# Optimization experiments

Hardware: AMD Instinct MI355X
Metric: run time of the kernel (lower is better)

Reference implementation:

```python
import jax, jax.numpy as jnp
import numpy as np

DIM = 192
NUM_HEADS = 6
WIN = (2, 7, 7)


def _relative_position_index(win):
    d, h, w = win
    coords = np.stack(np.meshgrid(np.arange(d), np.arange(h), np.arange(w), indexing='ij'))
    cf = coords.reshape(3, -1)  # (3, n)
    rel = cf[:, :, None] - cf[:, None, :]  # (3, n, n)
    rel = rel.transpose(1, 2, 0).copy()
    rel[:, :, 0] += d - 1
    rel[:, :, 1] += h - 1
    rel[:, :, 2] += w - 1
    rel[:, :, 0] *= (2 * h - 1) * (2 * w - 1)
    rel[:, :, 1] *= 2 * w - 1
    return rel.sum(-1).astype(np.int32)  # (n, n)


def setup_inputs() -> dict:
    key = jax.random.key(0)
    ks = jax.random.split(key, 8)
    n = WIN[0] * WIN[1] * WIN[2]  # 98
    table_size = (2 * WIN[0] - 1) * (2 * WIN[1] - 1) * (2 * WIN[2] - 1)  # 507
    b_ = 4096
    nW = 64
    x = jax.random.normal(ks[0], (b_, n, DIM), dtype=jnp.float32)
    mask = jax.random.normal(ks[1], (nW, n, n), dtype=jnp.float32)
    qkv_w = jax.random.normal(ks[2], (3 * DIM, DIM), dtype=jnp.float32) * (DIM ** -0.5)
    qkv_b = jnp.zeros((3 * DIM,), dtype=jnp.float32)
    proj_w = jax.random.normal(ks[3], (DIM, DIM), dtype=jnp.float32) * (DIM ** -0.5)
    proj_b = jnp.zeros((DIM,), dtype=jnp.float32)
    rpb_table = jax.random.normal(ks[4], (table_size, NUM_HEADS), dtype=jnp.float32) * 0.02
    rel_idx = jnp.asarray(_relative_position_index(WIN))  # (n, n) int32
    return {"x": x, "mask": mask, "qkv_w": qkv_w, "qkv_b": qkv_b,
            "proj_w": proj_w, "proj_b": proj_b, "rpb_table": rpb_table,
            "rel_idx": rel_idx}


def reference(x, mask, qkv_w, qkv_b, proj_w, proj_b, rpb_table, rel_idx):
    b_, n, c = x.shape
    H = NUM_HEADS
    hd = c // H
    scale = hd ** -0.5
    # QKV projection: (b_, n, 3, H, hd) -> (3, b_, H, n, hd)
    qkv = (x @ qkv_w.T + qkv_b).reshape(b_, n, 3, H, hd).transpose(2, 0, 3, 1, 4)
    q, k, v = qkv[0] * scale, qkv[1], qkv[2]
    attn = jnp.einsum('bhnd,bhmd->bhnm', q, k)
    # relative position bias gathered per (n, n) pair -> (H, n, n)
    bias = rpb_table[rel_idx]  # (n, n, H)
    attn = attn + bias.transpose(2, 0, 1)[None]
    # window mask add
    nW = mask.shape[0]
    attn = attn.reshape(b_ // nW, nW, H, n, n) + mask[None, :, None]
    attn = attn.reshape(b_, H, n, n)
    attn = jax.nn.softmax(attn, axis=-1)
    out = jnp.einsum('bhnm,bhmd->bhnd', attn, v)
    out = out.transpose(0, 2, 1, 3).reshape(b_, n, c)
    return out @ proj_w.T + proj_b
```

## Files before the change

### kernel.cpp

```cpp
#include <hip/hip_runtime.h>
#include <hip/hip_bf16.h>

#define NN 98
#define CC 192
#define NH 6
#define HDIM 32
#define NWIN 64
#define MPAD 100
#define NSTR 200
#define SWS 1920

#define WKV_ELEMS 73728
#define WQ_ELEMS  36864
#define WP_ELEMS  36864

typedef float f32x4 __attribute__((ext_vector_type(4)));
typedef __bf16 bf16x8 __attribute__((ext_vector_type(8)));
typedef __bf16 bf16x4 __attribute__((ext_vector_type(4)));

__device__ __forceinline__ f32x4 mfma_bf16(bf16x8 a, bf16x8 b, f32x4 c) {
  return __builtin_amdgcn_mfma_f32_16x16x32_bf16(a, b, c, 0, 0, 0);
}

__device__ __forceinline__ bf16x8 zero8() {
  bf16x8 z;
#pragma unroll
  for (int i = 0; i < 8; ++i) z[i] = (__bf16)0.0f;
  return z;
}

__device__ __forceinline__ float fast_exp2(float x) {
#if __has_builtin(__builtin_amdgcn_exp2f)
  return __builtin_amdgcn_exp2f(x);
#else
  return exp2f(x);
#endif
}

__device__ __forceinline__ bf16x8 ldlds8(const __bf16* p, int row, int k0) {
  int rc = row < NN ? row : (NN - 1);
  bf16x8 v = *(const bf16x8*)(p + rc * NSTR + k0);
  if (row >= NN) v = zero8();
  return v;
}

__global__ void prep_kernel(const float* __restrict__ mask,
                            const float* __restrict__ rpb,
                            const int* __restrict__ rel_idx,
                            const float* __restrict__ qkv_w,
                            const float* __restrict__ proj_w,
                            float* __restrict__ biasp,
                            float* __restrict__ maskp,
                            __bf16* __restrict__ wkvp,
                            __bf16* __restrict__ wqp,
                            __bf16* __restrict__ wpp) {
  const float LOG2E = 1.4426950408889634f;
  int i = blockIdx.x * 256 + threadIdx.x;
  if (i < NH * NN * MPAD) {
    int m = i % MPAD;
    int rem = i / MPAD;
    int n = rem % NN;
    int h = rem / NN;
    biasp[i] = (m < NN) ? rpb[rel_idx[n * NN + m] * NH + h] * LOG2E : -1e30f;
  }
  if (i < NWIN * NN * MPAD) {
    int m = i % MPAD;
    int rem = i / MPAD;
    int n = rem % NN;
    int wi = rem / NN;
    maskp[i] = (m < NN) ? mask[(wi * NN + n) * NN + m] * LOG2E : -1e30f;
  }
  if (i < WKV_ELEMS) {
    int j = i & 7;
    int lane = (i >> 3) & 63;
    int f = (i >> 9) & 3;
    int t = i >> 11;
    int ks = t % 6;
    int w = t / 6;
    int l15 = lane & 15, quad = lane >> 4;
    int row = (f < 2 ? CC : 2 * CC) + w * HDIM + (f & 1) * 16 + l15;
    int col = ks * 32 + quad * 8 + j;
    wkvp[i] = (__bf16)qkv_w[row * CC + col];
  }
  if (i < WQ_ELEMS) {
    int j = i & 7;
    int lane = (i >> 3) & 63;
    int f = (i >> 9) & 1;
    int t = i >> 10;
    int ks = t % 6;
    int w = t / 6;
    int l15 = lane & 15, quad = lane >> 4;
    int row = w * HDIM + f * 16 + l15;
    int col = ks * 32 + quad * 8 + j;
    wqp[i] = (__bf16)qkv_w[row * CC + col];
    wpp[i] = (__bf16)proj_w[row * CC + col];
  }
}

__global__ __launch_bounds__(384, 3) void attn_kernel(
    const float* __restrict__ x,
    const float* __restrict__ qkv_b,
    const float* __restrict__ proj_b,
    const float* __restrict__ biasp,
    const float* __restrict__ maskp,
    const __bf16* __restrict__ wkvp,
    const __bf16* __restrict__ wqp,
    const __bf16* __restrict__ wpp,
    float* __restrict__ out) {
  __shared__ alignas(16) __bf16 xs[NN * NSTR];
  __shared__ alignas(16) __bf16 stage[NH * SWS];

  const int b = blockIdx.x;
  const int tid = threadIdx.x;
  const int w = tid >> 6;
  const int lane = tid & 63;
  const int l15 = lane & 15;
  const int quad = lane >> 4;
  __bf16* st = stage + w * SWS;

  const float* xb = x + (size_t)b * (NN * CC);
  for (int i = tid; i < NN * CC / 4; i += 384) {
    int e = i * 4;
    int n = e / CC;
    int c = e - n * CC;
    f32x4 v = *(const f32x4*)(xb + e);
    bf16x4 p;
    p[0] = (__bf16)v[0]; p[1] = (__bf16)v[1]; p[2] = (__bf16)v[2]; p[3] = (__bf16)v[3];
    *(bf16x4*)&xs[n * NSTR + c] = p;
  }
  __syncthreads();

  f32x4 acc[2][7];

#pragma unroll
  for (int ct = 0; ct < 2; ++ct) {
    float bb = qkv_b[CC + w * HDIM + ct * 16 + l15];
#pragma unroll
    for (int rt = 0; rt < 7; ++rt) { f32x4 t = {bb, bb, bb, bb}; acc[ct][rt] = t; }
  }
  {
    const __bf16* wb = wkvp + (size_t)(w * 24) * 512 + lane * 8;
#pragma unroll
    for (int ks = 0; ks < 6; ++ks) {
      bf16x8 b0 = *(const bf16x8*)(wb + (ks * 4 + 0) * 512);
      bf16x8 b1 = *(const bf16x8*)(wb + (ks * 4 + 1) * 512);
      const int k0 = ks * 32 + quad * 8;
#pragma unroll
      for (int rt = 0; rt < 7; ++rt) {
        bf16x8 a = ldlds8(xs, rt * 16 + l15, k0);
        acc[0][rt] = mfma_bf16(a, b0, acc[0][rt]);
        acc[1][rt] = mfma_bf16(a, b1, acc[1][rt]);
      }
    }
  }

  bf16x8 ka[7];
#pragma unroll
  for (int rt = 0; rt < 7; ++rt) {
#pragma unroll
    for (int ct = 0; ct < 2; ++ct) {
      f32x4 v = acc[ct][rt];
      int hd = ct * 16 + l15;
#pragma unroll
      for (int r = 0; r < 4; ++r) st[(quad * 4 + r) * 40 + hd] = (__bf16)v[r];
    }
    bf16x8 f = *(const bf16x8*)&st[l15 * 40 + quad * 8];
    if (rt * 16 + l15 >= NN) f = zero8();
    ka[rt] = f;
  }

#pragma unroll
  for (int ct = 0; ct < 2; ++ct) {
    float bb = qkv_b[2 * CC + w * HDIM + ct * 16 + l15];
#pragma unroll
    for (int rt = 0; rt < 7; ++rt) { f32x4 t = {bb, bb, bb, bb}; acc[ct][rt] = t; }
  }
  {
    const __bf16* wb = wkvp + (size_t)(w * 24) * 512 + lane * 8;
#pragma unroll
    for (int ks = 0; ks < 6; ++ks) {
      bf16x8 b0 = *(const bf16x8*)(wb + (ks * 4 + 2) * 512);
      bf16x8 b1 = *(const bf16x8*)(wb + (ks * 4 + 3) * 512);
      const int k0 = ks * 32 + quad * 8;
#pragma unroll
      for (int rt = 0; rt < 7; ++rt) {
        bf16x8 a = ldlds8(xs, rt * 16 + l15, k0);
        acc[0][rt] = mfma_bf16(a, b0, acc[0][rt]);
        acc[1][rt] = mfma_bf16(a, b1, acc[1][rt]);
      }
    }
  }

  bf16x8 va[2][4];
#pragma unroll
  for (int ks = 0; ks < 4; ++ks) {
#pragma unroll
    for (int h2 = 0; h2 < 2; ++h2) {
      int rt = 2 * ks + h2;
      if (rt < 7) {
#pragma unroll
        for (int ct = 0; ct < 2; ++ct) {
          f32x4 v = acc[ct][rt];
          int d = ct * 16 + l15;
          int mloc = h2 * 16 + quad * 4;
          bf16x4 p;
#pragma unroll
          for (int r = 0; r < 4; ++r) p[r] = (__bf16)v[r];
          *(bf16x4*)&st[d * 40 + mloc] = p;
        }
      }
    }
#pragma unroll
    for (int dt = 0; dt < 2; ++dt) {
      bf16x8 f = *(const bf16x8*)&st[(dt * 16 + l15) * 40 + quad * 8];
      if (ks == 3 && quad >= 2) f = zero8();
      va[dt][ks] = f;
    }
  }

#pragma unroll
  for (int ct = 0; ct < 2; ++ct) {
    float bq = qkv_b[w * HDIM + ct * 16 + l15];
#pragma unroll
    for (int rt = 0; rt < 7; ++rt) { f32x4 t = {bq, bq, bq, bq}; acc[ct][rt] = t; }
  }
  {
    const __bf16* wb = wqp + (size_t)(w * 12) * 512 + lane * 8;
#pragma unroll
    for (int ks = 0; ks < 6; ++ks) {
      bf16x8 b0 = *(const bf16x8*)(wb + (ks * 2 + 0) * 512);
      bf16x8 b1 = *(const bf16x8*)(wb + (ks * 2 + 1) * 512);
      const int k0 = ks * 32 + quad * 8;
#pragma unroll
      for (int rt = 0; rt < 7; ++rt) {
        bf16x8 a = ldlds8(xs, rt * 16 + l15, k0);
        acc[0][rt] = mfma_bf16(a, b0, acc[0][rt]);
        acc[1][rt] = mfma_bf16(a, b1, acc[1][rt]);
      }
    }
  }

  const float qscale = 0.17677669529663687f * 1.4426950408889634f;
  bf16x8 qb[7];
#pragma unroll
  for (int rt = 0; rt < 7; ++rt) {
#pragma unroll
    for (int ct = 0; ct < 2; ++ct) {
      f32x4 v = acc[ct][rt];
      int hd = ct * 16 + l15;
#pragma unroll
      for (int r = 0; r < 4; ++r) st[(quad * 4 + r) * 40 + hd] = (__bf16)(v[r] * qscale);
    }
    bf16x8 f = *(const bf16x8*)&st[l15 * 40 + quad * 8];
    if (rt * 16 + l15 >= NN) f = zero8();
    qb[rt] = f;
  }

  __syncthreads();
  __bf16* O_lds = xs;

  const int wmask = b & (NWIN - 1);
#pragma unroll 1
  for (int nb = 0; nb < 7; ++nb) {
    const f32x4 z4 = {0.f, 0.f, 0.f, 0.f};
    f32x4 sacc[7];
#pragma unroll
    for (int mt = 0; mt < 7; ++mt) sacc[mt] = mfma_bf16(ka[mt], qb[nb], z4);

    int n = nb * 16 + l15;
    bool nvalid = (n < NN);
    int nc = nvalid ? n : 0;
    const float* bp = biasp + (size_t)(w * NN + nc) * MPAD;
    const float* mp = maskp + (size_t)(wmask * NN + nc) * MPAD;

    float mx = -3.0e38f;
#pragma unroll
    for (int mt = 0; mt < 7; ++mt) {
      int m0 = mt * 16 + quad * 4;
      bool ld = nvalid && (m0 < MPAD);
      f32x4 add = z4;
      if (ld) {
        f32x4 bm = *(const f32x4*)(bp + m0);
        f32x4 mm = *(const f32x4*)(mp + m0);
        add = bm + mm;
      }
#pragma unroll
      for (int r = 0; r < 4; ++r) {
        float v = ld ? (sacc[mt][r] + add[r]) : -1e30f;
        sacc[mt][r] = v;
        mx = fmaxf(mx, v);
      }
    }
    mx = fmaxf(mx, __shfl_xor(mx, 16, 64));
    mx = fmaxf(mx, __shfl_xor(mx, 32, 64));
    float sum = 0.f;
#pragma unroll
    for (int mt = 0; mt < 7; ++mt) {
#pragma unroll
      for (int r = 0; r < 4; ++r) {
        float p = fast_exp2(sacc[mt][r] - mx);
        sacc[mt][r] = p;
        sum += p;
      }
    }
    sum += __shfl_xor(sum, 16, 64);
    sum += __shfl_xor(sum, 32, 64);
    float rinv = 1.0f / sum;

#pragma unroll
    for (int mt = 0; mt < 7; ++mt) {
      bf16x4 p;
#pragma unroll
      for (int r = 0; r < 4; ++r) p[r] = (__bf16)sacc[mt][r];
      *(bf16x4*)&st[l15 * 120 + mt * 16 + quad * 4] = p;
    }
    bf16x8 pf[4];
#pragma unroll
    for (int ks = 0; ks < 4; ++ks) {
      bf16x8 f = *(const bf16x8*)&st[l15 * 120 + ks * 32 + quad * 8];
      if (ks == 3 && quad >= 2) f = zero8();
      pf[ks] = f;
    }

#pragma unroll
    for (int dt = 0; dt < 2; ++dt) {
      f32x4 o = z4;
#pragma unroll
      for (int ks = 0; ks < 4; ++ks) o = mfma_bf16(va[dt][ks], pf[ks], o);
      if (nvalid) {
        bf16x4 p;
#pragma unroll
        for (int r = 0; r < 4; ++r) p[r] = (__bf16)(o[r] * rinv);
        *(bf16x4*)&O_lds[n * NSTR + w * HDIM + dt * 16 + quad * 4] = p;
      }
    }
  }
  __syncthreads();

  f32x4 accP[2][7];
#pragma unroll
  for (int ct = 0; ct < 2; ++ct) {
    float pb = proj_b[w * HDIM + ct * 16 + l15];
#pragma unroll
    for (int rt = 0; rt < 7; ++rt) { f32x4 t = {pb, pb, pb, pb}; accP[ct][rt] = t; }
  }
  {
    const __bf16* wb = wpp + (size_t)(w * 12) * 512 + lane * 8;
#pragma unroll
    for (int ks = 0; ks < 6; ++ks) {
      bf16x8 b0 = *(const bf16x8*)(wb + (ks * 2 + 0) * 512);
      bf16x8 b1 = *(const bf16x8*)(wb + (ks * 2 + 1) * 512);
      const int k0 = ks * 32 + quad * 8;
#pragma unroll
      for (int rt = 0; rt < 7; ++rt) {
        bf16x8 a = ldlds8(O_lds, rt * 16 + l15, k0);
        accP[0][rt] = mfma_bf16(a, b0, accP[0][rt]);
        accP[1][rt] = mfma_bf16(a, b1, accP[1][rt]);
      }
    }
  }

  float* ob = out + (size_t)b * (NN * CC);
#pragma unroll
  for (int ct = 0; ct < 2; ++ct) {
    int cout = w * HDIM + ct * 16 + l15;
#pragma unroll
    for (int rt = 0; rt < 7; ++rt) {
      f32x4 v = accP[ct][rt];
#pragma unroll
      for (int r = 0; r < 4; ++r) {
        int n = rt * 16 + quad * 4 + r;
        if (n < NN) ob[n * CC + cout] = v[r];
      }
    }
  }
}

extern "C" void kernel_launch(void* const* d_in, const int* in_sizes, int n_in,
                              void* d_out, int out_size, void* d_ws, size_t ws_size,
                              hipStream_t stream) {
  const float* x = (const float*)d_in[0];
  const float* mask = (const float*)d_in[1];
  const float* qkv_w = (const float*)d_in[2];
  const float* qkv_b = (const float*)d_in[3];
  const float* proj_w = (const float*)d_in[4];
  const float* proj_b = (const float*)d_in[5];
  const float* rpb = (const float*)d_in[6];
  const int* rel_idx = (const int*)d_in[7];

  float* biasp = (float*)d_ws;
  float* maskp = biasp + NH * NN * MPAD;
  __bf16* wkvp = (__bf16*)(maskp + NWIN * NN * MPAD);
  __bf16* wqp = wkvp + WKV_ELEMS;
  __bf16* wpp = wqp + WQ_ELEMS;

  int prep_threads = NWIN * NN * MPAD;
  prep_kernel<<<(prep_threads + 255) / 256, 256, 0, stream>>>(
      mask, rpb, rel_idx, qkv_w, proj_w, biasp, maskp, wkvp, wqp, wpp);
  attn_kernel<<<4096, 384, 0, stream>>>(x, qkv_b, proj_b, biasp, maskp,
                                        wkvp, wqp, wpp, (float*)d_out);
}
```

Measured before the change: 1.562 ms.

## Pre-swizzle x into MFMA fragment layout and merge bias+mask table

Result: slower. 1.757 ms (+12.5%).

```diff
diff --git a/kernel.cpp b/kernel.cpp
--- a/kernel.cpp
+++ b/kernel.cpp
@@ -9,10 +9,12 @@
 #define MPAD 100
 #define NSTR 200
 #define SWS 1920
+#define NB 4096
 
 #define WKV_ELEMS 73728
 #define WQ_ELEMS  36864
-#define WP_ELEMS  36864
+#define COMB_ELEMS (NWIN * NH * NN * MPAD)
+#define XT_ELEMS ((size_t)NB * 42 * 512)
 
 typedef float f32x4 __attribute__((ext_vector_type(4)));
 typedef __bf16 bf16x8 __attribute__((ext_vector_type(8)));
@@ -37,38 +39,42 @@
 #endif
 }
 
-__device__ __forceinline__ bf16x8 ldlds8(const __bf16* p, int row, int k0) {
+__device__ __forceinline__ bf16x8 ldw8(const float* __restrict__ p) {
+  f32x4 a = *(const f32x4*)p;
+  f32x4 b = *(const f32x4*)(p + 4);
+  bf16x8 r;
+  r[0] = (__bf16)a[0]; r[1] = (__bf16)a[1]; r[2] = (__bf16)a[2]; r[3] = (__bf16)a[3];
+  r[4] = (__bf16)b[0]; r[5] = (__bf16)b[1]; r[6] = (__bf16)b[2]; r[7] = (__bf16)b[3];
+  return r;
+}
+
+__device__ __forceinline__ bf16x8 ldo(const __bf16* p, int row, int k0) {
   int rc = row < NN ? row : (NN - 1);
-  bf16x8 v = *(const bf16x8*)(p + rc * NSTR + k0);
-  if (row >= NN) v = zero8();
-  return v;
-}
-
-__global__ void prep_kernel(const float* __restrict__ mask,
-                            const float* __restrict__ rpb,
-                            const int* __restrict__ rel_idx,
-                            const float* __restrict__ qkv_w,
-                            const float* __restrict__ proj_w,
-                            float* __restrict__ biasp,
-                            float* __restrict__ maskp,
-                            __bf16* __restrict__ wkvp,
-                            __bf16* __restrict__ wqp,
-                            __bf16* __restrict__ wpp) {
+  return *(const bf16x8*)(p + rc * NSTR + k0);
+}
+
+__global__ void prep_small(const float* __restrict__ mask,
+                           const float* __restrict__ rpb,
+                           const int* __restrict__ rel_idx,
+                           const float* __restrict__ qkv_w,
+                           const float* __restrict__ proj_w,
+                           float* __restrict__ comb,
+                           __bf16* __restrict__ wkvp,
+                           __bf16* __restrict__ wqp,
+                           __bf16* __restrict__ wpp) {
   const float LOG2E = 1.4426950408889634f;
   int i = blockIdx.x * 256 + threadIdx.x;
-  if (i < NH * NN * MPAD) {
+  if (i < COMB_ELEMS) {
     int m = i % MPAD;
     int rem = i / MPAD;
     int n = rem % NN;
-    int h = rem / NN;
-    biasp[i] = (m < NN) ? rpb[rel_idx[n * NN + m] * NH + h] * LOG2E : -1e30f;
-  }
-  if (i < NWIN * NN * MPAD) {
-    int m = i % MPAD;
-    int rem = i / MPAD;
-    int n = rem % NN;
-    int wi = rem / NN;
-    maskp[i] = (m < NN) ? mask[(wi * NN + n) * NN + m] * LOG2E : -1e30f;
+    int rem2 = rem / NN;
+    int h = rem2 % NH;
+    int wi = rem2 / NH;
+    float v = -1e30f;
+    if (m < NN)
+      v = (rpb[rel_idx[n * NN + m] * NH + h] + mask[((size_t)wi * NN + n) * NN + m]) * LOG2E;
+    comb[i] = v;
   }
   if (i < WKV_ELEMS) {
     int j = i & 7;
@@ -97,17 +103,38 @@
   }
 }
 
+__global__ void prep_x(const float* __restrict__ x, __bf16* __restrict__ xt) {
+  int t = blockIdx.x * 256 + threadIdx.x;
+  int lane = t & 63;
+  int fid = t >> 6;
+  int rt = fid % 7;
+  int rem = fid / 7;
+  int ks = rem % 6;
+  int b = rem / 6;
+  int l15 = lane & 15, quad = lane >> 4;
+  int n = rt * 16 + l15;
+  bf16x8 v;
+  if (n < NN) {
+    const float* p = x + ((size_t)b * NN + n) * CC + ks * 32 + quad * 8;
+    v = ldw8(p);
+  } else {
+    v = zero8();
+  }
+  *(bf16x8*)&xt[(size_t)fid * 512 + lane * 8] = v;
+}
+
+template <bool XT>
 __global__ __launch_bounds__(384, 3) void attn_kernel(
     const float* __restrict__ x,
     const float* __restrict__ qkv_b,
     const float* __restrict__ proj_b,
-    const float* __restrict__ biasp,
-    const float* __restrict__ maskp,
+    const float* __restrict__ comb,
     const __bf16* __restrict__ wkvp,
     const __bf16* __restrict__ wqp,
     const __bf16* __restrict__ wpp,
+    const __bf16* __restrict__ xt,
     float* __restrict__ out) {
-  __shared__ alignas(16) __bf16 xs[NN * NSTR];
+  __shared__ alignas(16) __bf16 O_lds[NN * NSTR];
   __shared__ alignas(16) __bf16 stage[NH * SWS];
 
   const int b = blockIdx.x;
@@ -117,18 +144,8 @@
   const int l15 = lane & 15;
   const int quad = lane >> 4;
   __bf16* st = stage + w * SWS;
-
+  const __bf16* xtb = xt + (size_t)b * (42 * 512);
   const float* xb = x + (size_t)b * (NN * CC);
-  for (int i = tid; i < NN * CC / 4; i += 384) {
-    int e = i * 4;
-    int n = e / CC;
-    int c = e - n * CC;
-    f32x4 v = *(const f32x4*)(xb + e);
-    bf16x4 p;
-    p[0] = (__bf16)v[0]; p[1] = (__bf16)v[1]; p[2] = (__bf16)v[2]; p[3] = (__bf16)v[3];
-    *(bf16x4*)&xs[n * NSTR + c] = p;
-  }
-  __syncthreads();
 
   f32x4 acc[2][7];
 
@@ -144,10 +161,15 @@
     for (int ks = 0; ks < 6; ++ks) {
       bf16x8 b0 = *(const bf16x8*)(wb + (ks * 4 + 0) * 512);
       bf16x8 b1 = *(const bf16x8*)(wb + (ks * 4 + 1) * 512);
-      const int k0 = ks * 32 + quad * 8;
 #pragma unroll
       for (int rt = 0; rt < 7; ++rt) {
-        bf16x8 a = ldlds8(xs, rt * 16 + l15, k0);
+        bf16x8 a;
+        if (XT) {
+          a = *(const bf16x8*)&xtb[(ks * 7 + rt) * 512 + lane * 8];
+        } else {
+          int n = rt * 16 + l15;
+          a = (n < NN) ? ldw8(xb + n * CC + ks * 32 + quad * 8) : zero8();
+        }
         acc[0][rt] = mfma_bf16(a, b0, acc[0][rt]);
         acc[1][rt] = mfma_bf16(a, b1, acc[1][rt]);
       }
@@ -164,9 +186,7 @@
 #pragma unroll
       for (int r = 0; r < 4; ++r) st[(quad * 4 + r) * 40 + hd] = (__bf16)v[r];
     }
-    bf16x8 f = *(const bf16x8*)&st[l15 * 40 + quad * 8];
-    if (rt * 16 + l15 >= NN) f = zero8();
-    ka[rt] = f;
+    ka[rt] = *(const bf16x8*)&st[l15 * 40 + quad * 8];
   }
 
 #pragma unroll
@@ -181,10 +201,15 @@
     for (int ks = 0; ks < 6; ++ks) {
       bf16x8 b0 = *(const bf16x8*)(wb + (ks * 4 + 2) * 512);
       bf16x8 b1 = *(const bf16x8*)(wb + (ks * 4 + 3) * 512);
-      const int k0 = ks * 32 + quad * 8;
 #pragma unroll
       for (int rt = 0; rt < 7; ++rt) {
-        bf16x8 a = ldlds8(xs, rt * 16 + l15, k0);
+        bf16x8 a;
+        if (XT) {
+          a = *(const bf16x8*)&xtb[(ks * 7 + rt) * 512 + lane * 8];
+        } else {
+          int n = rt * 16 + l15;
+          a = (n < NN) ? ldw8(xb + n * CC + ks * 32 + quad * 8) : zero8();
+        }
         acc[0][rt] = mfma_bf16(a, b0, acc[0][rt]);
         acc[1][rt] = mfma_bf16(a, b1, acc[1][rt]);
       }
@@ -230,10 +255,15 @@
     for (int ks = 0; ks < 6; ++ks) {
       bf16x8 b0 = *(const bf16x8*)(wb + (ks * 2 + 0) * 512);
       bf16x8 b1 = *(const bf16x8*)(wb + (ks * 2 + 1) * 512);
-      const int k0 = ks * 32 + quad * 8;
 #pragma unroll
       for (int rt = 0; rt < 7; ++rt) {
-        bf16x8 a = ldlds8(xs, rt * 16 + l15, k0);
+        bf16x8 a;
+        if (XT) {
+          a = *(const bf16x8*)&xtb[(ks * 7 + rt) * 512 + lane * 8];
+        } else {
+          int n = rt * 16 + l15;
+          a = (n < NN) ? ldw8(xb + n * CC + ks * 32 + quad * 8) : zero8();
+        }
         acc[0][rt] = mfma_bf16(a, b0, acc[0][rt]);
         acc[1][rt] = mfma_bf16(a, b1, acc[1][rt]);
       }
@@ -251,42 +281,38 @@
 #pragma unroll
       for (int r = 0; r < 4; ++r) st[(quad * 4 + r) * 40 + hd] = (__bf16)(v[r] * qscale);
     }
-    bf16x8 f = *(const bf16x8*)&st[l15 * 40 + quad * 8];
-    if (rt * 16 + l15 >= NN) f = zero8();
-    qb[rt] = f;
-  }
-
-  __syncthreads();
-  __bf16* O_lds = xs;
+    qb[rt] = *(const bf16x8*)&st[l15 * 40 + quad * 8];
+  }
 
   const int wmask = b & (NWIN - 1);
+  const float* cbase = comb + (size_t)(wmask * NH + w) * NN * MPAD;
 #pragma unroll 1
   for (int nb = 0; nb < 7; ++nb) {
     const f32x4 z4 = {0.f, 0.f, 0.f, 0.f};
-    f32x4 sacc[7];
-#pragma unroll
-    for (int mt = 0; mt < 7; ++mt) sacc[mt] = mfma_bf16(ka[mt], qb[nb], z4);
+    const f32x4 neg4 = {-1e30f, -1e30f, -1e30f, -1e30f};
 
     int n = nb * 16 + l15;
     bool nvalid = (n < NN);
     int nc = nvalid ? n : 0;
-    const float* bp = biasp + (size_t)(w * NN + nc) * MPAD;
-    const float* mp = maskp + (size_t)(wmask * NN + nc) * MPAD;
-
-    float mx = -3.0e38f;
+    const float* cp = cbase + (size_t)nc * MPAD;
+
+    f32x4 addv[7];
 #pragma unroll
     for (int mt = 0; mt < 7; ++mt) {
       int m0 = mt * 16 + quad * 4;
-      bool ld = nvalid && (m0 < MPAD);
-      f32x4 add = z4;
-      if (ld) {
-        f32x4 bm = *(const f32x4*)(bp + m0);
-        f32x4 mm = *(const f32x4*)(mp + m0);
-        add = bm + mm;
-      }
+      addv[mt] = (m0 < MPAD) ? *(const f32x4*)(cp + m0) : neg4;
+    }
+
+    f32x4 sacc[7];
+#pragma unroll
+    for (int mt = 0; mt < 7; ++mt) sacc[mt] = mfma_bf16(ka[mt], qb[nb], z4);
+
+    float mx = -3.0e38f;
+#pragma unroll
+    for (int mt = 0; mt < 7; ++mt) {
 #pragma unroll
       for (int r = 0; r < 4; ++r) {
-        float v = ld ? (sacc[mt][r] + add[r]) : -1e30f;
+        float v = sacc[mt][r] + addv[mt][r];
         sacc[mt][r] = v;
         mx = fmaxf(mx, v);
       }
@@ -353,7 +379,7 @@
       const int k0 = ks * 32 + quad * 8;
 #pragma unroll
       for (int rt = 0; rt < 7; ++rt) {
-        bf16x8 a = ldlds8(O_lds, rt * 16 + l15, k0);
+        bf16x8 a = ldo(O_lds, rt * 16 + l15, k0);
         accP[0][rt] = mfma_bf16(a, b0, accP[0][rt]);
         accP[1][rt] = mfma_bf16(a, b1, accP[1][rt]);
       }
@@ -361,16 +387,15 @@
   }
 
   float* ob = out + (size_t)b * (NN * CC);
-#pragma unroll
-  for (int ct = 0; ct < 2; ++ct) {
-    int cout = w * HDIM + ct * 16 + l15;
-#pragma unroll
-    for (int rt = 0; rt < 7; ++rt) {
-      f32x4 v = accP[ct][rt];
-#pragma unroll
-      for (int r = 0; r < 4; ++r) {
-        int n = rt * 16 + quad * 4 + r;
-        if (n < NN) ob[n * CC + cout] = v[r];
+  const int c0 = w * HDIM + l15;
+#pragma unroll
+  for (int rt = 0; rt < 7; ++rt) {
+#pragma unroll
+    for (int r = 0; r < 4; ++r) {
+      int n = rt * 16 + quad * 4 + r;
+      if (n < NN) {
+        ob[n * CC + c0] = accP[0][rt][r];
+        ob[n * CC + c0 + 16] = accP[1][rt][r];
       }
     }
   }
@@ -388,15 +413,25 @@
   const float* rpb = (const float*)d_in[6];
   const int* rel_idx = (const int*)d_in[7];
 
-  float* biasp = (float*)d_ws;
-  float* maskp = biasp + NH * NN * MPAD;
-  __bf16* wkvp = (__bf16*)(maskp + NWIN * NN * MPAD);
+  float* comb = (float*)d_ws;
+  __bf16* wkvp = (__bf16*)(comb + COMB_ELEMS);
   __bf16* wqp = wkvp + WKV_ELEMS;
   __bf16* wpp = wqp + WQ_ELEMS;
-
-  int prep_threads = NWIN * NN * MPAD;
-  prep_kernel<<<(prep_threads + 255) / 256, 256, 0, stream>>>(
-      mask, rpb, rel_idx, qkv_w, proj_w, biasp, maskp, wkvp, wqp, wpp);
-  attn_kernel<<<4096, 384, 0, stream>>>(x, qkv_b, proj_b, biasp, maskp,
-                                        wkvp, wqp, wpp, (float*)d_out);
-}
+  __bf16* xt = wpp + WQ_ELEMS;
+
+  size_t needed = (size_t)COMB_ELEMS * 4 +
+                  (size_t)(WKV_ELEMS + 2 * WQ_ELEMS) * 2 +
+                  XT_ELEMS * 2;
+  bool use_xt = ws_size >= needed;
+
+  prep_small<<<(COMB_ELEMS + 255) / 256, 256, 0, stream>>>(
+      mask, rpb, rel_idx, qkv_w, proj_w, comb, wkvp, wqp, wpp);
+  if (use_xt) {
+    prep_x<<<(int)((XT_ELEMS / 8) / 256), 256, 0, stream>>>(x, xt);
+    attn_kernel<true><<<NB, 384, 0, stream>>>(x, qkv_b, proj_b, comb,
+                                              wkvp, wqp, wpp, xt, (float*)d_out);
+  } else {
+    attn_kernel<false><<<NB, 384, 0, stream>>>(x, qkv_b, proj_b, comb,
+                                               wkvp, wqp, wpp, xt, (float*)d_out);
+  }
+}
```
